# Kernel optimization log

Hardware: AMD Instinct MI355X
Metric: run time of the kernel (lower is better)

Reference implementation:

```python
import jax, jax.numpy as jnp
import numpy as np

EPS = 1e-12

def _l2n(x):
    # torch F.normalize(p=2, dim=0): x / max(||x||_2, eps)
    return x / jnp.maximum(jnp.linalg.norm(x), EPS)

def _gru_cell(x, h, Wi, Wh, bi, bh):
    # torch GRU cell math; Wi:(3H,Din), Wh:(3H,H)
    gi = Wi @ x + bi
    gh = Wh @ h + bh
    i_r, i_z, i_n = jnp.split(gi, 3)
    h_r, h_z, h_n = jnp.split(gh, 3)
    r = jax.nn.sigmoid(i_r + h_r)
    z = jax.nn.sigmoid(i_z + h_z)
    n = jnp.tanh(i_n + r * h_n)
    return (1.0 - z) * n + z * h

def setup_inputs() -> dict:
    key = jax.random.key(0)
    ks = jax.random.split(key, 20)
    m, n, T = 10, 10, 100
    H1, H2, HID = 1600, 400, 2000
    D_in, D_out = 2 * m + n, m * n
    f32 = jnp.float32
    inp = {
        'y': jax.random.normal(ks[0], (n, T), f32),
        'm1x_0': jax.random.normal(ks[1], (m,), f32),
        'F': jax.random.normal(ks[2], (m, m), f32) * 0.1,
        'Hm': jax.random.normal(ks[3], (n, m), f32) * 0.1,
        'h0': jax.random.normal(ks[4], (2, HID), f32),
        'W1': jax.random.normal(ks[5], (H1, D_in), f32) * 0.05,
        'b1': jax.random.normal(ks[6], (H1,), f32) * 0.05,
        'Wi0': jax.random.normal(ks[7], (3 * HID, H1), f32) * 0.02,
        'Wh0': jax.random.normal(ks[8], (3 * HID, HID), f32) * 0.02,
        'bi0': jax.random.normal(ks[9], (3 * HID,), f32) * 0.02,
        'bh0': jax.random.normal(ks[10], (3 * HID,), f32) * 0.02,
        'Wi1': jax.random.normal(ks[11], (3 * HID, HID), f32) * 0.02,
        'Wh1': jax.random.normal(ks[12], (3 * HID, HID), f32) * 0.02,
        'bi1': jax.random.normal(ks[13], (3 * HID,), f32) * 0.02,
        'bh1': jax.random.normal(ks[14], (3 * HID,), f32) * 0.02,
        'W2': jax.random.normal(ks[15], (H2, HID), f32) * 0.02,
        'b2': jax.random.normal(ks[16], (H2,), f32) * 0.02,
        'W3': jax.random.normal(ks[17], (D_out, H2), f32) * 0.01,
        'b3': jax.random.normal(ks[18], (D_out,), f32) * 0.01,
    }
    return inp

def reference(y, m1x_0, F, Hm, h0, W1, b1, Wi0, Wh0, bi0, bh0,
              Wi1, Wh1, bi1, bh1, W2, b2, W3, b3):
    n, T = y.shape
    m = m1x_0.shape[0]
    # first step uses obs_process_0 = h(f(m1x_0)) as y_previous surrogate
    y_prev0 = Hm @ (F @ m1x_0)
    carry0 = (m1x_0, jnp.zeros_like(m1x_0), m1x_0, y_prev0, h0[0], h0[1])

    def step(carry, yt):
        post, prev_post, prev_prior, y_prev, h1, h2 = carry
        prior = F @ post              # step_prior
        m1y = Hm @ prior
        f1 = _l2n(yt - y_prev)        # innovation diff feature
        f3 = _l2n(post - prev_post)   # posterior update feature
        f4 = _l2n(post - prev_prior)  # residual feature
        kin = jnp.concatenate([f1, f3, f4])  # (2m+n,)
        a = jax.nn.relu(W1 @ kin + b1)
        h1n = _gru_cell(a, h1, Wi0, Wh0, bi0, bh0)
        h2n = _gru_cell(h1n, h2, Wi1, Wh1, bi1, bh1)
        g = jax.nn.relu(W2 @ h2n + b2)
        KG = (W3 @ g + b3).reshape(m, n)
        dy = yt - m1y
        new_post = prior + KG @ dy
        return (new_post, post, prior, yt, h1n, h2n), new_post

    _, xs = jax.lax.scan(step, carry0, y.T)  # xs: (T, m)
    return xs.T  # (m, T)
```

## Files before the change

### kernel.cpp

```cpp
#include <hip/hip_runtime.h>
#include <math.h>

#define NB 256
#define NT 1024
#define NW 16
#define TT 100
#define MM 10
#define NN 10
#define HID 2000
#define H1 1600
#define H2 400
#define G3 6000
#define KP 2048
#define RPB 24

#define SCOPE_AGENT __HIP_MEMORY_SCOPE_AGENT

typedef _Float16 h2v __attribute__((ext_vector_type(2)));

__device__ __forceinline__ float sigf(float x) { return 1.f / (1.f + __expf(-x)); }
__device__ __forceinline__ float tanhfast(float x) { return 2.f / (1.f + __expf(-2.f * x)) - 1.f; }

__device__ __forceinline__ float ld_coh(const float* p) {
  return __hip_atomic_load(p, __ATOMIC_RELAXED, SCOPE_AGENT);
}
__device__ __forceinline__ void st_coh(float* p, float v) {
  __hip_atomic_store(p, v, __ATOMIC_RELAXED, SCOPE_AGENT);
}
__device__ __forceinline__ float2 ld_coh2(const float* p) {
  unsigned long long v = __hip_atomic_load((const unsigned long long*)p,
                                           __ATOMIC_RELAXED, SCOPE_AGENT);
  union { unsigned long long u; float2 f; } c; c.u = v; return c.f;
}
__device__ __forceinline__ void stage_coh(const float* __restrict__ src,
                                          float* __restrict__ dst, int n, int tid) {
  const int n2 = n >> 1;
  for (int j = tid; j < n2; j += NT) {
    float2 v = ld_coh2(src + 2 * j);
    dst[2 * j]     = v.x;
    dst[2 * j + 1] = v.y;
  }
}

__device__ __forceinline__ void gridbar(unsigned* flags, unsigned* release,
                                        unsigned ep, int tid, int blk) {
  __syncthreads();
  if (tid == 0)
    __hip_atomic_store(flags + blk * 16, ep, __ATOMIC_RELAXED, SCOPE_AGENT);
  if (blk == 0) {
    if (tid < NB) {
      while (__hip_atomic_load(flags + tid * 16, __ATOMIC_RELAXED, SCOPE_AGENT) < ep)
        __builtin_amdgcn_s_sleep(1);
    }
    __syncthreads();
    if (tid == 0)
      __hip_atomic_store(release, ep, __ATOMIC_RELAXED, SCOPE_AGENT);
  } else {
    if (tid == 0) {
      while (__hip_atomic_load(release, __ATOMIC_RELAXED, SCOPE_AGENT) < ep)
        __builtin_amdgcn_s_sleep(1);
    }
  }
  __syncthreads();
}

template<int K>
__device__ __forceinline__ float rowdotT(const float* __restrict__ row,
                                         const float* __restrict__ x, int ln) {
  constexpr int NFULL = K / 256;
  constexpr int REM   = K - NFULL * 256;
  const int base = ln * 4;
  float4 w[NFULL + (REM ? 1 : 0)];
  #pragma unroll
  for (int i = 0; i < NFULL; ++i)
    w[i] = *reinterpret_cast<const float4*>(row + base + i * 256);
  bool tail = false;
  if constexpr (REM != 0) {
    tail = (base + NFULL * 256 + 3 < K);
    if (tail) w[NFULL] = *reinterpret_cast<const float4*>(row + base + NFULL * 256);
  }
  float acc = 0.f;
  #pragma unroll
  for (int i = 0; i < NFULL; ++i) {
    const float4 xv = *reinterpret_cast<const float4*>(x + base + i * 256);
    acc = fmaf(w[i].x, xv.x, acc);
    acc = fmaf(w[i].y, xv.y, acc);
    acc = fmaf(w[i].z, xv.z, acc);
    acc = fmaf(w[i].w, xv.w, acc);
  }
  if constexpr (REM != 0) {
    if (tail) {
      const float4 xv = *reinterpret_cast<const float4*>(x + base + NFULL * 256);
      acc = fmaf(w[NFULL].x, xv.x, acc);
      acc = fmaf(w[NFULL].y, xv.y, acc);
      acc = fmaf(w[NFULL].z, xv.z, acc);
      acc = fmaf(w[NFULL].w, xv.w, acc);
    }
  }
  #pragma unroll
  for (int off = 32; off; off >>= 1) acc += __shfl_xor(acc, off, 64);
  return acc;
}

__device__ __forceinline__ void sweep24(const _Float16* __restrict__ W,
                                        const float* __restrict__ bias,
                                        int row0, int nrows,
                                        const _Float16* __restrict__ xh,
                                        float* __restrict__ outw,
                                        bool relu,
                                        int wv, int ln, int tid, float* red,
                                        float* __restrict__ gloc)
{
  const _Float16* wp = W + (size_t)row0 * KP + wv * 3072 + ln * 8;
  uint4 w[6];
  #pragma unroll
  for (int c = 0; c < 6; ++c)
    w[c] = *reinterpret_cast<const uint4*>(wp + c * 512);
  float a0 = 0.f, a1 = 0.f;
  const int first = (3 * wv) >> 1;
  #pragma unroll
  for (int c = 0; c < 6; ++c) {
    const int flat = wv * 3072 + c * 512;
    const int sel  = (flat >> 11) - first;
    const int col  = (flat & (KP - 1)) + ln * 8;
    const uint4 xv = *reinterpret_cast<const uint4*>(xh + col);
    union { uint4 u; h2v h[4]; } wu, xu;
    wu.u = w[c]; xu.u = xv;
    float acc = sel ? a1 : a0;
    #pragma unroll
    for (int q = 0; q < 4; ++q)
      acc = __builtin_amdgcn_fdot2(wu.h[q], xu.h[q], acc, false);
    if (sel) a1 = acc; else a0 = acc;
  }
  #pragma unroll
  for (int off = 32; off; off >>= 1) {
    a0 += __shfl_xor(a0, off, 64);
    a1 += __shfl_xor(a1, off, 64);
  }
  __syncthreads();
  if (ln == 0) { red[wv * 2] = a0; red[wv * 2 + 1] = a1; }
  __syncthreads();
  if (tid < nrows) {
    const int k = tid / 3, m = tid % 3;
    float v = (m == 0) ? red[4 * k]
            : (m == 1) ? red[4 * k + 1] + red[4 * k + 2]
                       : red[4 * k + 3];
    v += bias[row0 + tid];
    if (relu) v = fmaxf(v, 0.f);
    if (gloc) gloc[tid] = v;
    st_coh(outw + row0 + tid, v);
  }
}

__global__ __launch_bounds__(256)
void convh(const float* __restrict__ src, _Float16* __restrict__ dst,
           int rows, int K, int padrows) {
  const size_t total = (size_t)padrows * KP;
  for (size_t i = (size_t)blockIdx.x * blockDim.x + threadIdx.x; i < total;
       i += (size_t)gridDim.x * blockDim.x) {
    const int r = (int)(i >> 11), c = (int)(i & (KP - 1));
    float v = (r < rows && c < K) ? src[(size_t)r * K + c] : 0.f;
    dst[i] = (_Float16)v;
  }
}
__global__ __launch_bounds__(256)
void convw1(const float* __restrict__ src, _Float16* __restrict__ dst) {
  const int i = blockIdx.x * 256 + threadIdx.x;
  const int r = i >> 5, c = i & 31;
  float v = (r < H1 && c < 30) ? src[r * 30 + c] : 0.f;
  dst[i] = (_Float16)v;
}

__global__ __launch_bounds__(NT)
void knet_f16(const float* __restrict__ y, const float* __restrict__ m1x0,
              const float* __restrict__ F, const float* __restrict__ Hm,
              const float* __restrict__ h0,
              const float* __restrict__ W1, const float* __restrict__ b1,
              const float* __restrict__ Wi0, const float* __restrict__ Wh0,
              const float* __restrict__ bi0, const float* __restrict__ bh0,
              const float* __restrict__ Wi1, const float* __restrict__ Wh1,
              const float* __restrict__ bi1, const float* __restrict__ bh1,
              const float* __restrict__ W2, const float* __restrict__ b2,
              const float* __restrict__ W3, const float* __restrict__ b3,
              float* __restrict__ out, float* __restrict__ ws)
{
  const int blk = blockIdx.x, tid = threadIdx.x;
  const int wv = tid >> 6, ln = tid & 63;

  float* a_ws    = ws;
  float* gi0_ws  = ws + 1600;
  float* gh0_ws  = ws + 7600;
  float* gi1_ws  = ws + 13600;
  float* gh1_ws  = ws + 19600;
  float* g_ws    = ws + 25600;
  float* vpart_ws = ws + 26000;
  unsigned* flags   = (unsigned*)(ws + 27712);
  unsigned* release = flags + NB * 16;

  const _Float16* whbase = (const _Float16*)((const char*)ws + 131072);
  const _Float16* Wi0h = whbase;
  const _Float16* Wh0h = whbase + (size_t)G3 * KP;
  const _Float16* Wi1h = whbase + (size_t)2 * G3 * KP;
  const _Float16* Wh1h = whbase + (size_t)3 * G3 * KP;
  const _Float16* W2h  = whbase + (size_t)4 * G3 * KP;
  const _Float16* W1h  = whbase + (size_t)4 * G3 * KP + (size_t)408 * KP;

  __shared__ __align__(16) _Float16 ah[KP];
  __shared__ __align__(16) _Float16 h1h[KP];
  __shared__ __align__(16) _Float16 h2h[KP];
  __shared__ __align__(16) float h1l[HID];
  __shared__ __align__(16) float h2l[HID];
  __shared__ __align__(16) float xs[1728];
  __shared__ __align__(16) _Float16 kin_h[32];
  __shared__ float red[32];
  __shared__ float gloc_s[RPB];
  __shared__ float post_s[MM], prevpost_s[MM], prevprior_s[MM], prior_s[MM];
  __shared__ float dy_s[NN], yprev_s[NN], tmp_s[MM];
  __shared__ float d1_s[NN], d3_s[MM], d4_s[MM];
  __shared__ float kin_s[32], nrm_s[3];
  __shared__ float v_s[MM * NN], np_s[MM];

  for (int j = tid; j < HID; j += NT) {
    float v1 = h0[j], v2 = h0[HID + j];
    h1l[j] = v1; h2l[j] = v2;
    h1h[j] = (_Float16)v1; h2h[j] = (_Float16)v2;
  }
  for (int j = HID + tid; j < KP; j += NT) { h1h[j] = (_Float16)0.f; h2h[j] = (_Float16)0.f; }
  for (int j = H1 + tid; j < KP; j += NT) ah[j] = (_Float16)0.f;
  __syncthreads();

  unsigned ep = 0;

  for (int t = 0; t < TT; ++t) {
    if (blk == NB - 1) {
      if (t > 0) {
        stage_coh(vpart_ws, xs, 1700, tid);
        __syncthreads();
        if (tid < MM * NN) {
          float s = b3[tid];
          #pragma unroll
          for (int k = 0; k < 17; ++k) s += xs[k * 100 + tid];
          v_s[tid] = s;
        }
        __syncthreads();
        if (tid < MM) {
          float np = prior_s[tid];
          #pragma unroll
          for (int j = 0; j < NN; ++j) np = fmaf(v_s[tid * NN + j], dy_s[j], np);
          out[tid * TT + (t - 1)] = np;
          np_s[tid] = np;
        }
        __syncthreads();
        if (tid < MM) {
          prevpost_s[tid]  = post_s[tid];
          prevprior_s[tid] = prior_s[tid];
          post_s[tid]      = np_s[tid];
        }
        __syncthreads();
      } else {
        if (tid < MM) {
          post_s[tid]      = m1x0[tid];
          prevpost_s[tid]  = 0.f;
          prevprior_s[tid] = m1x0[tid];
          float tv = 0.f;
          for (int j = 0; j < MM; ++j) tv = fmaf(F[tid * MM + j], m1x0[j], tv);
          tmp_s[tid] = tv;
        }
        __syncthreads();
        if (tid < NN) {
          float yp = 0.f;
          for (int j = 0; j < MM; ++j) yp = fmaf(Hm[tid * MM + j], tmp_s[j], yp);
          yprev_s[tid] = yp;
        }
        __syncthreads();
      }
      if (tid < MM) {
        float pr = 0.f;
        for (int j = 0; j < MM; ++j) pr = fmaf(F[tid * MM + j], post_s[j], pr);
        prior_s[tid] = pr;
      }
      __syncthreads();
      if (tid < NN) {
        float my = 0.f;
        for (int j = 0; j < MM; ++j) my = fmaf(Hm[tid * MM + j], prior_s[j], my);
        float yt = y[tid * TT + t];
        dy_s[tid] = yt - my;
        d1_s[tid] = yt - ((t == 0) ? yprev_s[tid] : y[tid * TT + (t - 1)]);
        d3_s[tid] = post_s[tid] - prevpost_s[tid];
        d4_s[tid] = post_s[tid] - prevprior_s[tid];
      }
      __syncthreads();
      if (tid == 0) {
        float n1 = 0.f, n3 = 0.f, n4 = 0.f;
        for (int j = 0; j < NN; ++j) n1 += d1_s[j] * d1_s[j];
        for (int j = 0; j < MM; ++j) { n3 += d3_s[j] * d3_s[j]; n4 += d4_s[j] * d4_s[j]; }
        nrm_s[0] = fmaxf(sqrtf(n1), 1e-12f);
        nrm_s[1] = fmaxf(sqrtf(n3), 1e-12f);
        nrm_s[2] = fmaxf(sqrtf(n4), 1e-12f);
      }
      __syncthreads();
      if (tid < NN) kin_s[tid] = d1_s[tid] / nrm_s[0];
      if (tid < MM) {
        kin_s[NN + tid]      = d3_s[tid] / nrm_s[1];
        kin_s[NN + MM + tid] = d4_s[tid] / nrm_s[2];
      }
      __syncthreads();
      if (tid < 32) kin_h[tid] = (_Float16)((tid < 30) ? kin_s[tid] : 0.f);
      __syncthreads();
      if (tid < 800) {
        const _Float16* wp = W1h + (size_t)tid * 64;
        uint4 q[8];
        #pragma unroll
        for (int c = 0; c < 8; ++c)
          q[c] = *reinterpret_cast<const uint4*>(wp + c * 8);
        const uint4* kq = reinterpret_cast<const uint4*>(kin_h);
        union { uint4 u; h2v h[4]; } kk[4], qq;
        #pragma unroll
        for (int c = 0; c < 4; ++c) kk[c].u = kq[c];
        const int r0 = 2 * tid;
        float s0 = b1[r0], s1 = b1[r0 + 1];
        #pragma unroll
        for (int c = 0; c < 4; ++c) {
          qq.u = q[c];
          #pragma unroll
          for (int p = 0; p < 4; ++p)
            s0 = __builtin_amdgcn_fdot2(qq.h[p], kk[c].h[p], s0, false);
        }
        #pragma unroll
        for (int c = 0; c < 4; ++c) {
          qq.u = q[c + 4];
          #pragma unroll
          for (int p = 0; p < 4; ++p)
            s1 = __builtin_amdgcn_fdot2(qq.h[p], kk[c].h[p], s1, false);
        }
        st_coh(a_ws + r0,     fmaxf(s0, 0.f));
        st_coh(a_ws + r0 + 1, fmaxf(s1, 0.f));
      }
    } else if (blk < 250) {
      sweep24(Wh1h, bh1, RPB * blk, RPB, h2h, gh1_ws, false, wv, ln, tid, red, nullptr);
      if (t == 0) {
        sweep24(Wh0h, bh0, RPB * blk, RPB, h1h, gh0_ws, false, wv, ln, tid, red, nullptr);
      }
    } else {
      sweep24(Wh0h, bh0, RPB * (blk - 250), RPB, h1h, gh0_ws, false, wv, ln, tid, red, nullptr);
    }
    ++ep; gridbar(flags, release, ep, tid, blk);

    if (blk < 250) {
      const int n2 = H1 >> 1;
      for (int j = tid; j < n2; j += NT) {
        float2 v = ld_coh2(a_ws + 2 * j);
        ah[2 * j]     = (_Float16)v.x;
        ah[2 * j + 1] = (_Float16)v.y;
      }
      __syncthreads();
      sweep24(Wi0h, bi0, RPB * blk, RPB, ah, gi0_ws, false, wv, ln, tid, red, nullptr);
    } else {
      sweep24(Wh0h, bh0, RPB * (blk - 245), RPB, h1h, gh0_ws, false, wv, ln, tid, red, nullptr);
    }
    ++ep; gridbar(flags, release, ep, tid, blk);

    {
      for (int j = tid; j < HID / 2; j += NT) {
        float2 ir = ld_coh2(gi0_ws + 2 * j),            hr = ld_coh2(gh0_ws + 2 * j);
        float2 iz = ld_coh2(gi0_ws + HID + 2 * j),      hz = ld_coh2(gh0_ws + HID + 2 * j);
        float2 in_ = ld_coh2(gi0_ws + 2 * HID + 2 * j), hn = ld_coh2(gh0_ws + 2 * HID + 2 * j);
        float r0 = sigf(ir.x + hr.x), r1 = sigf(ir.y + hr.y);
        float z0 = sigf(iz.x + hz.x), z1 = sigf(iz.y + hz.y);
        float n0 = tanhfast(in_.x + r0 * hn.x), n1 = tanhfast(in_.y + r1 * hn.y);
        float o0 = (1.f - z0) * n0 + z0 * h1l[2 * j];
        float o1 = (1.f - z1) * n1 + z1 * h1l[2 * j + 1];
        h1l[2 * j] = o0; h1l[2 * j + 1] = o1;
        h1h[2 * j] = (_Float16)o0; h1h[2 * j + 1] = (_Float16)o1;
      }
      __syncthreads();
      if (blk < 250)
        sweep24(Wi1h, bi1, RPB * blk, RPB, h1h, gi1_ws, false, wv, ln, tid, red, nullptr);
    }
    ++ep; gridbar(flags, release, ep, tid, blk);

    {
      for (int j = tid; j < HID / 2; j += NT) {
        float2 ir = ld_coh2(gi1_ws + 2 * j),            hr = ld_coh2(gh1_ws + 2 * j);
        float2 iz = ld_coh2(gi1_ws + HID + 2 * j),      hz = ld_coh2(gh1_ws + HID + 2 * j);
        float2 in_ = ld_coh2(gi1_ws + 2 * HID + 2 * j), hn = ld_coh2(gh1_ws + 2 * HID + 2 * j);
        float r0 = sigf(ir.x + hr.x), r1 = sigf(ir.y + hr.y);
        float z0 = sigf(iz.x + hz.x), z1 = sigf(iz.y + hz.y);
        float n0 = tanhfast(in_.x + r0 * hn.x), n1 = tanhfast(in_.y + r1 * hn.y);
        float o0 = (1.f - z0) * n0 + z0 * h2l[2 * j];
        float o1 = (1.f - z1) * n1 + z1 * h2l[2 * j + 1];
        h2l[2 * j] = o0; h2l[2 * j + 1] = o1;
        h2h[2 * j] = (_Float16)o0; h2h[2 * j + 1] = (_Float16)o1;
      }
      __syncthreads();
      if (blk < 239) {
        sweep24(Wh0h, bh0, RPB * (blk + 11), RPB, h1h, gh0_ws, false, wv, ln, tid, red, nullptr);
      } else {
        const int task = blk - 239;
        const int row0 = RPB * task;
        const int nr = (H2 - row0 < RPB) ? (H2 - row0) : RPB;
        sweep24(W2h, b2, row0, nr, h2h, g_ws, true, wv, ln, tid, red, gloc_s);
        __syncthreads();
        if (tid < MM * NN) {
          float s = 0.f;
          const float* w3c = W3 + (size_t)tid * H2 + row0;
          for (int j = 0; j < nr; ++j) s = fmaf(w3c[j], gloc_s[j], s);
          st_coh(vpart_ws + task * 100 + tid, s);
        }
      }
    }
    ++ep; gridbar(flags, release, ep, tid, blk);
  }

  if (blk == NB - 1) {
    stage_coh(vpart_ws, xs, 1700, tid);
    __syncthreads();
    if (tid < MM * NN) {
      float s = b3[tid];
      #pragma unroll
      for (int k = 0; k < 17; ++k) s += xs[k * 100 + tid];
      v_s[tid] = s;
    }
    __syncthreads();
    if (tid < MM) {
      float np = prior_s[tid];
      #pragma unroll
      for (int j = 0; j < NN; ++j) np = fmaf(v_s[tid * NN + j], dy_s[j], np);
      out[tid * TT + (TT - 1)] = np;
    }
  }
}

__global__ __launch_bounds__(NT)
void knet_f32(const float* __restrict__ y, const float* __restrict__ m1x0,
              const float* __restrict__ F, const float* __restrict__ Hm,
              const float* __restrict__ h0,
              const float* __restrict__ W1, const float* __restrict__ b1,
              const float* __restrict__ Wi0, const float* __restrict__ Wh0,
              const float* __restrict__ bi0, const float* __restrict__ bh0,
              const float* __restrict__ Wi1, const float* __restrict__ Wh1,
              const float* __restrict__ bi1, const float* __restrict__ bh1,
              const float* __restrict__ W2, const float* __restrict__ b2,
              const float* __restrict__ W3, const float* __restrict__ b3,
              float* __restrict__ out, float* __restrict__ ws)
{
  const int blk = blockIdx.x, tid = threadIdx.x;
  const int wv = tid >> 6, ln = tid & 63;

  float* a_ws   = ws;
  float* gi0_ws = ws + 1600;
  float* gh0_ws = ws + 7600;
  float* gi1_ws = ws + 13600;
  float* gh1_ws = ws + 19600;
  float* g_ws   = ws + 25600;
  unsigned* flags   = (unsigned*)(ws + 26624);
  unsigned* release = flags + NB * 16;

  __shared__ __align__(16) float xs[1664];
  __shared__ __align__(16) float h1l[HID];
  __shared__ __align__(16) float h2l[HID];
  __shared__ float post_s[MM], prevpost_s[MM], prevprior_s[MM], prior_s[MM];
  __shared__ float dy_s[NN], yprev_s[NN], tmp_s[MM];
  __shared__ float d1_s[NN], d3_s[MM], d4_s[MM];
  __shared__ float kin_s[32], nrm_s[3];
  __shared__ float v_s[MM * NN], np_s[MM];

  for (int j = tid; j < HID; j += NT) { h1l[j] = h0[j]; h2l[j] = h0[HID + j]; }
  __syncthreads();

  unsigned ep = 0;

  for (int t = 0; t < TT; ++t) {
    if (blk == NB - 1) {
      if (t > 0) {
        stage_coh(g_ws, xs, H2, tid);
        __syncthreads();
        for (int r = wv; r < MM * NN; r += NW) {
          float acc = rowdotT<H2>(W3 + (size_t)r * H2, xs, ln);
          if (ln == 0) v_s[r] = acc + b3[r];
        }
        __syncthreads();
        if (tid < MM) {
          float np = prior_s[tid];
          #pragma unroll
          for (int j = 0; j < NN; ++j) np = fmaf(v_s[tid * NN + j], dy_s[j], np);
          out[tid * TT + (t - 1)] = np;
          np_s[tid] = np;
        }
        __syncthreads();
        if (tid < MM) {
          prevpost_s[tid]  = post_s[tid];
          prevprior_s[tid] = prior_s[tid];
          post_s[tid]      = np_s[tid];
        }
        __syncthreads();
      } else {
        if (tid < MM) {
          post_s[tid]      = m1x0[tid];
          prevpost_s[tid]  = 0.f;
          prevprior_s[tid] = m1x0[tid];
          float tv = 0.f;
          for (int j = 0; j < MM; ++j) tv = fmaf(F[tid * MM + j], m1x0[j], tv);
          tmp_s[tid] = tv;
        }
        __syncthreads();
        if (tid < NN) {
          float yp = 0.f;
          for (int j = 0; j < MM; ++j) yp = fmaf(Hm[tid * MM + j], tmp_s[j], yp);
          yprev_s[tid] = yp;
        }
        __syncthreads();
      }
      if (tid < MM) {
        float pr = 0.f;
        for (int j = 0; j < MM; ++j) pr = fmaf(F[tid * MM + j], post_s[j], pr);
        prior_s[tid] = pr;
      }
      __syncthreads();
      if (tid < NN) {
        float my = 0.f;
        for (int j = 0; j < MM; ++j) my = fmaf(Hm[tid * MM + j], prior_s[j], my);
        float yt = y[tid * TT + t];
        dy_s[tid] = yt - my;
        d1_s[tid] = yt - ((t == 0) ? yprev_s[tid] : y[tid * TT + (t - 1)]);
        d3_s[tid] = post_s[tid] - prevpost_s[tid];
        d4_s[tid] = post_s[tid] - prevprior_s[tid];
      }
      __syncthreads();
      if (tid == 0) {
        float n1 = 0.f, n3 = 0.f, n4 = 0.f;
        for (int j = 0; j < NN; ++j) n1 += d1_s[j] * d1_s[j];
        for (int j = 0; j < MM; ++j) { n3 += d3_s[j] * d3_s[j]; n4 += d4_s[j] * d4_s[j]; }
        nrm_s[0] = fmaxf(sqrtf(n1), 1e-12f);
        nrm_s[1] = fmaxf(sqrtf(n3), 1e-12f);
        nrm_s[2] = fmaxf(sqrtf(n4), 1e-12f);
      }
      __syncthreads();
      if (tid < NN) kin_s[tid] = d1_s[tid] / nrm_s[0];
      if (tid < MM) {
        kin_s[NN + tid]      = d3_s[tid] / nrm_s[1];
        kin_s[NN + MM + tid] = d4_s[tid] / nrm_s[2];
      }
      __syncthreads();
      for (int r = tid; r < H1; r += NT) {
        float acc = b1[r];
        const float* row = W1 + (size_t)r * 30;
        #pragma unroll
        for (int k = 0; k < 30; ++k) acc = fmaf(row[k], kin_s[k], acc);
        st_coh(a_ws + r, fmaxf(acc, 0.f));
      }
    } else {
      const int gw = blk * NW + wv;
      for (int r = gw; r < G3; r += (NB - 1) * NW) {
        float acc = rowdotT<HID>(Wh1 + (size_t)r * HID, h2l, ln);
        if (ln == 0) st_coh(gh1_ws + r, acc + bh1[r]);
      }
      if (t == 0) {
        for (int r = gw; r < G3; r += (NB - 1) * NW) {
          float acc = rowdotT<HID>(Wh0 + (size_t)r * HID, h1l, ln);
          if (ln == 0) st_coh(gh0_ws + r, acc + bh0[r]);
        }
      }
    }
    ++ep; gridbar(flags, release, ep, tid, blk);

    stage_coh(a_ws, xs, H1, tid);
    __syncthreads();
    {
      const int gw = blk * NW + wv;
      for (int r = gw; r < G3; r += NB * NW) {
        float acc = rowdotT<H1>(Wi0 + (size_t)r * H1, xs, ln);
        if (ln == 0) st_coh(gi0_ws + r, acc + bi0[r]);
      }
    }
    ++ep; gridbar(flags, release, ep, tid, blk);

    {
      for (int j = tid; j < HID / 2; j += NT) {
        float2 ir = ld_coh2(gi0_ws + 2 * j),            hr = ld_coh2(gh0_ws + 2 * j);
        float2 iz = ld_coh2(gi0_ws + HID + 2 * j),      hz = ld_coh2(gh0_ws + HID + 2 * j);
        float2 in_ = ld_coh2(gi0_ws + 2 * HID + 2 * j), hn = ld_coh2(gh0_ws + 2 * HID + 2 * j);
        float r0 = sigf(ir.x + hr.x), r1 = sigf(ir.y + hr.y);
        float z0 = sigf(iz.x + hz.x), z1 = sigf(iz.y + hz.y);
        float n0 = tanhfast(in_.x + r0 * hn.x), n1 = tanhfast(in_.y + r1 * hn.y);
        h1l[2 * j]     = (1.f - z0) * n0 + z0 * h1l[2 * j];
        h1l[2 * j + 1] = (1.f - z1) * n1 + z1 * h1l[2 * j + 1];
      }
      __syncthreads();
      const int gw = blk * NW + wv;
      for (int r = gw; r < G3; r += NB * NW) {
        float acc = rowdotT<HID>(Wi1 + (size_t)r * HID, h1l, ln);
        if (ln == 0) st_coh(gi1_ws + r, acc + bi1[r]);
      }
    }
    ++ep; gridbar(flags, release, ep, tid, blk);

    {
      for (int j = tid; j < HID / 2; j += NT) {
        float2 ir = ld_coh2(gi1_ws + 2 * j),            hr = ld_coh2(gh1_ws + 2 * j);
        float2 iz = ld_coh2(gi1_ws + HID + 2 * j),      hz = ld_coh2(gh1_ws + HID + 2 * j);
        float2 in_ = ld_coh2(gi1_ws + 2 * HID + 2 * j), hn = ld_coh2(gh1_ws + 2 * HID + 2 * j);
        float r0 = sigf(ir.x + hr.x), r1 = sigf(ir.y + hr.y);
        float z0 = sigf(iz.x + hz.x), z1 = sigf(iz.y + hz.y);
        float n0 = tanhfast(in_.x + r0 * hn.x), n1 = tanhfast(in_.y + r1 * hn.y);
        h2l[2 * j]     = (1.f - z0) * n0 + z0 * h2l[2 * j];
        h2l[2 * j + 1] = (1.f - z1) * n1 + z1 * h2l[2 * j + 1];
      }
      __syncthreads();
      const int gw = blk * NW + wv;
      for (int r = gw; r < H2 + G3; r += NB * NW) {
        if (r < H2) {
          float acc = rowdotT<HID>(W2 + (size_t)r * HID, h2l, ln);
          if (ln == 0) st_coh(g_ws + r, fmaxf(acc + b2[r], 0.f));
        } else {
          const int rr = r - H2;
          float acc = rowdotT<HID>(Wh0 + (size_t)rr * HID, h1l, ln);
          if (ln == 0) st_coh(gh0_ws + rr, acc + bh0[rr]);
        }
      }
    }
    ++ep; gridbar(flags, release, ep, tid, blk);
  }

  if (blk == NB - 1) {
    stage_coh(g_ws, xs, H2, tid);
    __syncthreads();
    for (int r = wv; r < MM * NN; r += NW) {
      float acc = rowdotT<H2>(W3 + (size_t)r * H2, xs, ln);
      if (ln == 0) v_s[r] = acc + b3[r];
    }
    __syncthreads();
    if (tid < MM) {
      float np = prior_s[tid];
      #pragma unroll
      for (int j = 0; j < NN; ++j) np = fmaf(v_s[tid * NN + j], dy_s[j], np);
      out[tid * TT + (TT - 1)] = np;
    }
  }
}

extern "C" void kernel_launch(void* const* d_in, const int* in_sizes, int n_in,
                              void* d_out, int out_size, void* d_ws, size_t ws_size,
                              hipStream_t stream) {
  const float* y    = (const float*)d_in[0];
  const float* m1x0 = (const float*)d_in[1];
  const float* F    = (const float*)d_in[2];
  const float* Hm   = (const float*)d_in[3];
  const float* h0   = (const float*)d_in[4];
  const float* W1   = (const float*)d_in[5];
  const float* b1   = (const float*)d_in[6];
  const float* Wi0  = (const float*)d_in[7];
  const float* Wh0  = (const float*)d_in[8];
  const float* bi0  = (const float*)d_in[9];
  const float* bh0  = (const float*)d_in[10];
  const float* Wi1  = (const float*)d_in[11];
  const float* Wh1  = (const float*)d_in[12];
  const float* bi1  = (const float*)d_in[13];
  const float* bh1  = (const float*)d_in[14];
  const float* W2   = (const float*)d_in[15];
  const float* b2   = (const float*)d_in[16];
  const float* W3   = (const float*)d_in[17];
  const float* b3   = (const float*)d_in[18];
  float* out = (float*)d_out;
  float* ws  = (float*)d_ws;

  const size_t NEED = 131072 +
      ((size_t)4 * G3 * KP + (size_t)408 * KP + (size_t)65536) * 2;

  void* args[] = { &y, &m1x0, &F, &Hm, &h0, &W1, &b1, &Wi0, &Wh0, &bi0, &bh0,
                   &Wi1, &Wh1, &bi1, &bh1, &W2, &b2, &W3, &b3, &out, &ws };

  if (ws_size >= NEED) {
    hipMemsetAsync((char*)d_ws + 110848, 0, NB * 64 + 64, stream);
    _Float16* wh = (_Float16*)((char*)d_ws + 131072);
    convh<<<2048, 256, 0, stream>>>(Wi0, wh,                         G3, H1,  G3);
    convh<<<2048, 256, 0, stream>>>(Wh0, wh + (size_t)G3 * KP,       G3, HID, G3);
    convh<<<2048, 256, 0, stream>>>(Wi1, wh + (size_t)2 * G3 * KP,   G3, HID, G3);
    convh<<<2048, 256, 0, stream>>>(Wh1, wh + (size_t)3 * G3 * KP,   G3, HID, G3);
    convh<<<2048, 256, 0, stream>>>(W2,  wh + (size_t)4 * G3 * KP,   H2, HID, 408);
    convw1<<<256, 256, 0, stream>>>(W1,  wh + (size_t)4 * G3 * KP + (size_t)408 * KP);
    hipLaunchCooperativeKernel((const void*)knet_f16, dim3(NB), dim3(NT),
                               args, 0, stream);
  } else {
    hipMemsetAsync((char*)d_ws + 26624 * sizeof(float), 0, NB * 64 + 64, stream);
    hipLaunchCooperativeKernel((const void*)knet_f32, dim3(NB), dim3(NT),
                               args, 0, stream);
  }
}
```

Measured before the change: 3.760 ms.

## Cut grid barriers per step from four to two with flags and double-buffered gh1

Restructures the per-timestep schedule of the persistent cooperative kernel so that each step uses two grid-wide barriers instead of four. The layer-2 GRU update and the W2/W3 head are deferred into the next step and computed redundantly per block. Point-to-point flags (aflag for the W1 output, vflag for the head partials) replace full barriers where only a producer-consumer relation exists, and gh1 is double-buffered to avoid races. The intent is to cut barrier latency on a latency-bound recurrent loop. In exchange it adds redundant elementwise work, a rebalanced task assignment, and more complex ordering that could hide races.

```diff
diff --git a/kernel.cpp b/kernel.cpp
--- a/kernel.cpp
+++ b/kernel.cpp
@@ -60,6 +60,18 @@
       while (__hip_atomic_load(release, __ATOMIC_RELAXED, SCOPE_AGENT) < ep)
         __builtin_amdgcn_s_sleep(1);
     }
+  }
+  __syncthreads();
+}
+
+__device__ __forceinline__ void set_flag(unsigned* f, unsigned v, int tid) {
+  __syncthreads();
+  if (tid == 0) __hip_atomic_store(f, v, __ATOMIC_RELAXED, SCOPE_AGENT);
+}
+__device__ __forceinline__ void wait_flag(const unsigned* f, unsigned v, int tid) {
+  if (tid == 0) {
+    while (__hip_atomic_load(f, __ATOMIC_RELAXED, SCOPE_AGENT) < v)
+      __builtin_amdgcn_s_sleep(1);
   }
   __syncthreads();
 }
@@ -187,17 +199,19 @@
   const int blk = blockIdx.x, tid = threadIdx.x;
   const int wv = tid >> 6, ln = tid & 63;
 
-  float* a_ws    = ws;
-  float* gi0_ws  = ws + 1600;
-  float* gh0_ws  = ws + 7600;
-  float* gi1_ws  = ws + 13600;
-  float* gh1_ws  = ws + 19600;
-  float* g_ws    = ws + 25600;
-  float* vpart_ws = ws + 26000;
-  unsigned* flags   = (unsigned*)(ws + 27712);
-  unsigned* release = flags + NB * 16;
-
-  const _Float16* whbase = (const _Float16*)((const char*)ws + 131072);
+  float* a_ws     = ws;
+  float* gi0_ws   = ws + 1600;
+  float* gh0_ws   = ws + 7600;
+  float* gi1_ws   = ws + 13600;
+  float* gh1b     = ws + 19600;
+  float* g_ws     = ws + 31600;
+  float* vpart_ws = ws + 32000;
+  unsigned* flags   = (unsigned*)(ws + 33728);
+  unsigned* release = flags + 256 * 16;
+  unsigned* vflag   = release + 16;
+  unsigned* aflag   = vflag + 17 * 16;
+
+  const _Float16* whbase = (const _Float16*)((const char*)ws + 152576);
   const _Float16* Wi0h = whbase;
   const _Float16* Wh0h = whbase + (size_t)G3 * KP;
   const _Float16* Wi1h = whbase + (size_t)2 * G3 * KP;
@@ -232,8 +246,16 @@
   unsigned ep = 0;
 
   for (int t = 0; t < TT; ++t) {
+    float* gh1w = gh1b + (t & 1) * G3;
+    float* gh1r = gh1b + ((t + 1) & 1) * G3;
+
     if (blk == NB - 1) {
       if (t > 0) {
+        if (tid < 17) {
+          while (__hip_atomic_load(vflag + tid * 16, __ATOMIC_RELAXED, SCOPE_AGENT) < (unsigned)t)
+            __builtin_amdgcn_s_sleep(1);
+        }
+        __syncthreads();
         stage_coh(vpart_ws, xs, 1700, tid);
         __syncthreads();
         if (tid < MM * NN) {
@@ -336,31 +358,65 @@
         st_coh(a_ws + r0,     fmaxf(s0, 0.f));
         st_coh(a_ws + r0 + 1, fmaxf(s1, 0.f));
       }
-    } else if (blk < 250) {
-      sweep24(Wh1h, bh1, RPB * blk, RPB, h2h, gh1_ws, false, wv, ln, tid, red, nullptr);
-      if (t == 0) {
-        sweep24(Wh0h, bh0, RPB * blk, RPB, h1h, gh0_ws, false, wv, ln, tid, red, nullptr);
-      }
+      set_flag(aflag, (unsigned)(t + 1), tid);
     } else {
-      sweep24(Wh0h, bh0, RPB * (blk - 250), RPB, h1h, gh0_ws, false, wv, ln, tid, red, nullptr);
+      if (blk >= 17) {
+        if (blk <= 249) {
+          sweep24(Wh0h, bh0, RPB * (blk - 17), RPB, h1h, gh0_ws, false, wv, ln, tid, red, nullptr);
+        } else {
+          #pragma unroll
+          for (int i = 0; i < 4; ++i) {
+            const int task = 233 + (blk - 250) + 5 * i;
+            if (task < 250)
+              sweep24(Wh0h, bh0, RPB * task, RPB, h1h, gh0_ws, false, wv, ln, tid, red, nullptr);
+          }
+        }
+      }
+      if (t > 0) {
+        for (int j = tid; j < HID / 2; j += NT) {
+          float2 ir = ld_coh2(gi1_ws + 2 * j),            hr = ld_coh2(gh1r + 2 * j);
+          float2 iz = ld_coh2(gi1_ws + HID + 2 * j),      hz = ld_coh2(gh1r + HID + 2 * j);
+          float2 in_ = ld_coh2(gi1_ws + 2 * HID + 2 * j), hn = ld_coh2(gh1r + 2 * HID + 2 * j);
+          float r0 = sigf(ir.x + hr.x), r1 = sigf(ir.y + hr.y);
+          float z0 = sigf(iz.x + hz.x), z1 = sigf(iz.y + hz.y);
+          float n0 = tanhfast(in_.x + r0 * hn.x), n1 = tanhfast(in_.y + r1 * hn.y);
+          float o0 = (1.f - z0) * n0 + z0 * h2l[2 * j];
+          float o1 = (1.f - z1) * n1 + z1 * h2l[2 * j + 1];
+          h2l[2 * j] = o0; h2l[2 * j + 1] = o1;
+          h2h[2 * j] = (_Float16)o0; h2h[2 * j + 1] = (_Float16)o1;
+        }
+        __syncthreads();
+        if (blk < 17) {
+          const int row0 = RPB * blk;
+          const int nr = (H2 - row0 < RPB) ? (H2 - row0) : RPB;
+          sweep24(W2h, b2, row0, nr, h2h, g_ws, true, wv, ln, tid, red, gloc_s);
+          __syncthreads();
+          if (tid < MM * NN) {
+            float s = 0.f;
+            const float* w3c = W3 + (size_t)tid * H2 + row0;
+            for (int j = 0; j < nr; ++j) s = fmaf(w3c[j], gloc_s[j], s);
+            st_coh(vpart_ws + blk * 100 + tid, s);
+          }
+          set_flag(vflag + blk * 16, (unsigned)t, tid);
+        }
+      }
+      if (blk <= 249)
+        sweep24(Wh1h, bh1, RPB * blk, RPB, h2h, gh1w, false, wv, ln, tid, red, nullptr);
+      if (blk <= 249) {
+        wait_flag(aflag, (unsigned)(t + 1), tid);
+        const int n2 = H1 >> 1;
+        for (int j = tid; j < n2; j += NT) {
+          float2 v = ld_coh2(a_ws + 2 * j);
+          ah[2 * j]     = (_Float16)v.x;
+          ah[2 * j + 1] = (_Float16)v.y;
+        }
+        __syncthreads();
+        sweep24(Wi0h, bi0, RPB * blk, RPB, ah, gi0_ws, false, wv, ln, tid, red, nullptr);
+      }
     }
     ++ep; gridbar(flags, release, ep, tid, blk);
 
-    if (blk < 250) {
-      const int n2 = H1 >> 1;
-      for (int j = tid; j < n2; j += NT) {
-        float2 v = ld_coh2(a_ws + 2 * j);
-        ah[2 * j]     = (_Float16)v.x;
-        ah[2 * j + 1] = (_Float16)v.y;
-      }
-      __syncthreads();
-      sweep24(Wi0h, bi0, RPB * blk, RPB, ah, gi0_ws, false, wv, ln, tid, red, nullptr);
-    } else {
-      sweep24(Wh0h, bh0, RPB * (blk - 245), RPB, h1h, gh0_ws, false, wv, ln, tid, red, nullptr);
-    }
-    ++ep; gridbar(flags, release, ep, tid, blk);
-
-    {
+    if (blk != NB - 1) {
       for (int j = tid; j < HID / 2; j += NT) {
         float2 ir = ld_coh2(gi0_ws + 2 * j),            hr = ld_coh2(gh0_ws + 2 * j);
         float2 iz = ld_coh2(gi0_ws + HID + 2 * j),      hz = ld_coh2(gh0_ws + HID + 2 * j);
@@ -374,45 +430,44 @@
         h1h[2 * j] = (_Float16)o0; h1h[2 * j + 1] = (_Float16)o1;
       }
       __syncthreads();
-      if (blk < 250)
+      if (blk <= 249)
         sweep24(Wi1h, bi1, RPB * blk, RPB, h1h, gi1_ws, false, wv, ln, tid, red, nullptr);
     }
     ++ep; gridbar(flags, release, ep, tid, blk);
-
-    {
-      for (int j = tid; j < HID / 2; j += NT) {
-        float2 ir = ld_coh2(gi1_ws + 2 * j),            hr = ld_coh2(gh1_ws + 2 * j);
-        float2 iz = ld_coh2(gi1_ws + HID + 2 * j),      hz = ld_coh2(gh1_ws + HID + 2 * j);
-        float2 in_ = ld_coh2(gi1_ws + 2 * HID + 2 * j), hn = ld_coh2(gh1_ws + 2 * HID + 2 * j);
-        float r0 = sigf(ir.x + hr.x), r1 = sigf(ir.y + hr.y);
-        float z0 = sigf(iz.x + hz.x), z1 = sigf(iz.y + hz.y);
-        float n0 = tanhfast(in_.x + r0 * hn.x), n1 = tanhfast(in_.y + r1 * hn.y);
-        float o0 = (1.f - z0) * n0 + z0 * h2l[2 * j];
-        float o1 = (1.f - z1) * n1 + z1 * h2l[2 * j + 1];
-        h2l[2 * j] = o0; h2l[2 * j + 1] = o1;
-        h2h[2 * j] = (_Float16)o0; h2h[2 * j + 1] = (_Float16)o1;
-      }
-      __syncthreads();
-      if (blk < 239) {
-        sweep24(Wh0h, bh0, RPB * (blk + 11), RPB, h1h, gh0_ws, false, wv, ln, tid, red, nullptr);
-      } else {
-        const int task = blk - 239;
-        const int row0 = RPB * task;
-        const int nr = (H2 - row0 < RPB) ? (H2 - row0) : RPB;
-        sweep24(W2h, b2, row0, nr, h2h, g_ws, true, wv, ln, tid, red, gloc_s);
-        __syncthreads();
-        if (tid < MM * NN) {
-          float s = 0.f;
-          const float* w3c = W3 + (size_t)tid * H2 + row0;
-          for (int j = 0; j < nr; ++j) s = fmaf(w3c[j], gloc_s[j], s);
-          st_coh(vpart_ws + task * 100 + tid, s);
-        }
-      }
-    }
-    ++ep; gridbar(flags, release, ep, tid, blk);
-  }
-
+  }
+
+  if (blk < 17) {
+    float* gh1r = gh1b + ((TT + 1) & 1) * G3;
+    for (int j = tid; j < HID / 2; j += NT) {
+      float2 ir = ld_coh2(gi1_ws + 2 * j),            hr = ld_coh2(gh1r + 2 * j);
+      float2 iz = ld_coh2(gi1_ws + HID + 2 * j),      hz = ld_coh2(gh1r + HID + 2 * j);
+      float2 in_ = ld_coh2(gi1_ws + 2 * HID + 2 * j), hn = ld_coh2(gh1r + 2 * HID + 2 * j);
+      float r0 = sigf(ir.x + hr.x), r1 = sigf(ir.y + hr.y);
+      float z0 = sigf(iz.x + hz.x), z1 = sigf(iz.y + hz.y);
+      float n0 = tanhfast(in_.x + r0 * hn.x), n1 = tanhfast(in_.y + r1 * hn.y);
+      float o0 = (1.f - z0) * n0 + z0 * h2l[2 * j];
+      float o1 = (1.f - z1) * n1 + z1 * h2l[2 * j + 1];
+      h2h[2 * j] = (_Float16)o0; h2h[2 * j + 1] = (_Float16)o1;
+    }
+    __syncthreads();
+    const int row0 = RPB * blk;
+    const int nr = (H2 - row0 < RPB) ? (H2 - row0) : RPB;
+    sweep24(W2h, b2, row0, nr, h2h, g_ws, true, wv, ln, tid, red, gloc_s);
+    __syncthreads();
+    if (tid < MM * NN) {
+      float s = 0.f;
+      const float* w3c = W3 + (size_t)tid * H2 + row0;
+      for (int j = 0; j < nr; ++j) s = fmaf(w3c[j], gloc_s[j], s);
+      st_coh(vpart_ws + blk * 100 + tid, s);
+    }
+    set_flag(vflag + blk * 16, (unsigned)TT, tid);
+  }
   if (blk == NB - 1) {
+    if (tid < 17) {
+      while (__hip_atomic_load(vflag + tid * 16, __ATOMIC_RELAXED, SCOPE_AGENT) < (unsigned)TT)
+        __builtin_amdgcn_s_sleep(1);
+    }
+    __syncthreads();
     stage_coh(vpart_ws, xs, 1700, tid);
     __syncthreads();
     if (tid < MM * NN) {
@@ -664,15 +719,16 @@
   float* out = (float*)d_out;
   float* ws  = (float*)d_ws;
 
-  const size_t NEED = 131072 +
+  const size_t WBASE = 152576;
+  const size_t NEED = WBASE +
       ((size_t)4 * G3 * KP + (size_t)408 * KP + (size_t)65536) * 2;
 
   void* args[] = { &y, &m1x0, &F, &Hm, &h0, &W1, &b1, &Wi0, &Wh0, &bi0, &bh0,
                    &Wi1, &Wh1, &bi1, &bh1, &W2, &b2, &W3, &b3, &out, &ws };
 
   if (ws_size >= NEED) {
-    hipMemsetAsync((char*)d_ws + 110848, 0, NB * 64 + 64, stream);
-    _Float16* wh = (_Float16*)((char*)d_ws + 131072);
+    hipMemsetAsync((char*)d_ws + 33728 * sizeof(float), 0, 275 * 64, stream);
+    _Float16* wh = (_Float16*)((char*)d_ws + WBASE);
     convh<<<2048, 256, 0, stream>>>(Wi0, wh,                         G3, H1,  G3);
     convh<<<2048, 256, 0, stream>>>(Wh0, wh + (size_t)G3 * KP,       G3, HID, G3);
     convh<<<2048, 256, 0, stream>>>(Wi1, wh + (size_t)2 * G3 * KP,   G3, HID, G3);
```

New measurement: 3.733 ms. No clear change (-0.7%).
